# Optimization experiments

Measured on AMD Instinct MI355X. Metric: run time of the kernel, lower is better.

The kernel has to match this reference:

```python
import jax, jax.numpy as jnp
import numpy as np
import math

N, E, NF, BF, H, NH, DEPTH = 2048, 65536, 128, 16, 512, 8, 5
HD = H // NH

def _lin(key, fan_in, fan_out):
    k1, k2 = jax.random.split(key)
    W = jax.random.normal(k1, (fan_in, fan_out), jnp.float32) * math.sqrt(2.0 / fan_out)
    b = jnp.zeros((fan_out,), jnp.float32)
    return W, b

def setup_inputs() -> dict:
    key = jax.random.key(0)
    ks = jax.random.split(key, 12)
    x = jax.random.normal(ks[0], (N, NF), jnp.float32)
    edge_index = jax.random.randint(ks[1], (2, E), 0, N, jnp.int64)
    edge_attr = jax.random.normal(ks[2], (E, BF), jnp.float32)
    Wn, bn = _lin(ks[3], NF, H)
    We, be = _lin(ks[4], BF, NH)
    Wq, bq = _lin(ks[5], H, H)
    Wk, bk = _lin(ks[6], H, H)
    Wv, bv = _lin(ks[7], H, H)
    Wo, bo = _lin(ks[8], H, H)
    W1, b1 = _lin(ks[9], H, 4 * H)
    W2, b2 = _lin(ks[10], 4 * H, H)
    g1 = jnp.ones((H,), jnp.float32); be1 = jnp.zeros((H,), jnp.float32)
    g2 = jnp.ones((H,), jnp.float32); be2 = jnp.zeros((H,), jnp.float32)
    return dict(x=x, edge_index=edge_index, edge_attr=edge_attr,
                Wn=Wn, bn=bn, We=We, be=be, Wq=Wq, bq=bq, Wk=Wk, bk=bk,
                Wv=Wv, bv=bv, Wo=Wo, bo=bo, W1=W1, b1=b1, W2=W2, b2=b2,
                g1=g1, be1=be1, g2=g2, be2=be2)

def _ln(x, g, b, eps=1e-5):
    m = jnp.mean(x, axis=-1, keepdims=True)
    v = jnp.var(x, axis=-1, keepdims=True)
    return (x - m) * jax.lax.rsqrt(v + eps) * g + b

def reference(x, edge_index, edge_attr, Wn, bn, We, be, Wq, bq, Wk, bk,
              Wv, bv, Wo, bo, W1, b1, W2, b2, g1, be1, g2, be2):
    h = x @ Wn + bn                                   # [N, H]
    e_bias = edge_attr @ We + be                      # [E, NH]
    src, dst = edge_index[0], edge_index[1]
    bias = jnp.zeros((NH, N, N), jnp.float32).at[:, src, dst].set(e_bias.T)
    scale = 1.0 / math.sqrt(HD)
    for _ in range(DEPTH):
        Q = (h @ Wq + bq).reshape(N, NH, HD).transpose(1, 0, 2)   # [h, n, d]
        K = (h @ Wk + bk).reshape(N, NH, HD).transpose(1, 0, 2)
        V = (h @ Wv + bv).reshape(N, NH, HD).transpose(1, 0, 2)
        scores = jnp.einsum('hnd,hmd->hnm', Q, K) * scale + bias  # [h, n, m]
        attn = jax.nn.softmax(scores, axis=-1)
        out = jnp.einsum('hnm,hmd->hnd', attn, V)                 # [h, n, d]
        out = out.transpose(1, 0, 2).reshape(N, H) @ Wo + bo
        h = _ln(h + out, g1, be1)
        h_ff = jnp.maximum(h @ W1 + b1, 0.0) @ W2 + b2
        h = _ln(h + h_ff, g2, be2)
    return h
```

## Files before the change

### kernel.cpp

```cpp
#include <hip/hip_runtime.h>
#include <hip/hip_bf16.h>

#define NN 2048
#define EE 65536
#define NF_ 128
#define HH 512
#define NHH 8
#define HD 64
#define DEPTH 5
#define KSPLIT 2
#define KEYS_PER (NN / KSPLIT)
#define NTILE (KEYS_PER / 64)
#define NTILE_TOT (NN / 64)
#define LOG2E 1.4426950408889634f

typedef __attribute__((ext_vector_type(8))) short bf16x8;
typedef __attribute__((ext_vector_type(4))) float f32x4;

__device__ __forceinline__ ushort f2bf(float x) {
    uint u = __builtin_bit_cast(uint, x);
    u += 0x7fffu + ((u >> 16) & 1u);
    return (ushort)(u >> 16);
}

#define GLD16(gp, lp)                                                          \
    __builtin_amdgcn_global_load_lds(                                          \
        (const __attribute__((address_space(1))) unsigned int*)(gp),           \
        (__attribute__((address_space(3))) unsigned int*)(lp), 16, 0, 0)

__device__ __forceinline__ void bar_lgkm() {
    asm volatile("s_waitcnt lgkmcnt(0)" ::: "memory");
    __builtin_amdgcn_s_barrier();
    __builtin_amdgcn_sched_barrier(0);
}
__device__ __forceinline__ void bar_vm(int pk) {
    if (pk) asm volatile("s_waitcnt vmcnt(2) lgkmcnt(0)" ::: "memory");
    else    asm volatile("s_waitcnt vmcnt(0) lgkmcnt(0)" ::: "memory");
    __builtin_amdgcn_s_barrier();
    __builtin_amdgcn_sched_barrier(0);
}

template<int BM, int BN, int OUT, int RELU>
__global__ __launch_bounds__(256) void gemm_mfma(const ushort* __restrict__ A,
                                                 const ushort* __restrict__ Bt,
                                                 const float* __restrict__ bias,
                                                 float* __restrict__ C,
                                                 ushort* __restrict__ Cb,
                                                 ushort* __restrict__ qb,
                                                 ushort* __restrict__ kb,
                                                 ushort* __restrict__ vtb,
                                                 int M, int N, int K) {
    constexpr int WM = BM / 2, WN = BN / 2;
    constexpr int MR = BM / 32, NR = BN / 32;
    __shared__ __align__(16) ushort As[2][BM * 64];
    __shared__ __align__(16) ushort Bs[2][BN * 64];
    const int t = threadIdx.x;
    const int w = t >> 6, l = t & 63;
    const int wr = w >> 1, wc = w & 1;
    const int m0 = blockIdx.y * BM, n0 = blockIdx.x * BN;

    f32x4 acc[MR][NR];
#pragma unroll
    for (int m = 0; m < MR; ++m)
#pragma unroll
        for (int n = 0; n < NR; ++n) acc[m][n] = (f32x4){0.f, 0.f, 0.f, 0.f};

    const int srow = t >> 3, sch = t & 7;
    auto stage = [&](int buf, int kt) {
#pragma unroll
        for (int r = 0; r < MR; ++r) {
            int rr = r * 32 + srow;
            int c = sch ^ (rr & 7);
            GLD16(A + (size_t)(m0 + rr) * K + kt * 64 + c * 8,
                  &As[buf][rr * 64 + sch * 8]);
        }
#pragma unroll
        for (int r = 0; r < NR; ++r) {
            int rr = r * 32 + srow;
            int c = sch ^ (rr & 7);
            GLD16(Bt + (size_t)(n0 + rr) * K + kt * 64 + c * 8,
                  &Bs[buf][rr * 64 + sch * 8]);
        }
    };

    stage(0, 0);
    const int NT = K / 64;
    for (int kt = 0; kt < NT; ++kt) {
        __syncthreads();
        if (kt + 1 < NT) stage((kt + 1) & 1, kt + 1);
        const int buf = kt & 1;
#pragma unroll
        for (int kk = 0; kk < 2; ++kk) {
            bf16x8 af[MR], bfr[NR];
#pragma unroll
            for (int m = 0; m < MR; ++m) {
                int R = wr * WM + m * 16 + (l & 15);
                int c = kk * 4 + (l >> 4);
                af[m] = *(const bf16x8*)&As[buf][R * 64 + (c ^ (R & 7)) * 8];
            }
#pragma unroll
            for (int n = 0; n < NR; ++n) {
                int R = wc * WN + n * 16 + (l & 15);
                int c = kk * 4 + (l >> 4);
                bfr[n] = *(const bf16x8*)&Bs[buf][R * 64 + (c ^ (R & 7)) * 8];
            }
#pragma unroll
            for (int m = 0; m < MR; ++m)
#pragma unroll
                for (int n = 0; n < NR; ++n)
                    acc[m][n] = __builtin_amdgcn_mfma_f32_16x16x32_bf16(af[m], bfr[n], acc[m][n], 0, 0, 0);
        }
    }

#pragma unroll
    for (int m = 0; m < MR; ++m) {
        int row = m0 + wr * WM + m * 16 + (l >> 4) * 4;
#pragma unroll
        for (int n = 0; n < NR; ++n) {
            int col = n0 + wc * WN + n * 16 + (l & 15);
            float bv = bias[col];
#pragma unroll
            for (int j = 0; j < 4; ++j) {
                float vv = acc[m][n][j] + bv;
                if (RELU) vv = fmaxf(vv, 0.f);
                int r = row + j;
                if (OUT == 0) {
                    C[(size_t)r * N + col] = vv;
                } else if (OUT == 1) {
                    C[(size_t)r * N + col] = vv;
                    Cb[(size_t)r * N + col] = f2bf(vv);
                } else if (OUT == 2) {
                    Cb[(size_t)r * N + col] = f2bf(vv);
                } else {
                    int type = col >> 9, head = (col >> 6) & 7, dd = col & 63;
                    ushort bv16 = f2bf(vv);
                    if (type == 0) qb[((size_t)head * NN + r) * 64 + dd] = bv16;
                    else if (type == 1) kb[((size_t)head * NN + r) * 64 + dd] = bv16;
                    else vtb[((size_t)head * 64 + dd) * NN + r] = bv16;
                }
            }
        }
    }
}

__global__ __launch_bounds__(256) void xcvt(const float* __restrict__ x, ushort* __restrict__ xb, int n) {
    int i = blockIdx.x * 256 + threadIdx.x;
    if (i < n) xb[i] = f2bf(x[i]);
}

__global__ __launch_bounds__(256) void wtrans(const float* __restrict__ W, ushort* __restrict__ WT,
                                              int K, int N, int rowoff) {
    __shared__ float tile[32][33];
    int n0 = blockIdx.x * 32, k0 = blockIdx.y * 32;
    int tc = threadIdx.x & 31, tr = threadIdx.x >> 5;
#pragma unroll
    for (int i = 0; i < 32; i += 8) tile[tr + i][tc] = W[(size_t)(k0 + tr + i) * N + n0 + tc];
    __syncthreads();
#pragma unroll
    for (int i = 0; i < 32; i += 8)
        WT[(size_t)(rowoff + n0 + tr + i) * K + k0 + tc] = f2bf(tile[tc][tr + i]);
}

__global__ __launch_bounds__(256) void bconcat(const float* __restrict__ a, const float* __restrict__ b,
                                               const float* __restrict__ c, float* __restrict__ o) {
    int i = blockIdx.x * 256 + threadIdx.x;
    if (i < 1536) o[i] = i < 512 ? a[i] : (i < 1024 ? b[i - 512] : c[i - 1024]);
}

__global__ __launch_bounds__(256) void ebias_kernel(const float* __restrict__ ea,
                                                    const float* __restrict__ We,
                                                    const float* __restrict__ be,
                                                    float* __restrict__ eb) {
    int e = blockIdx.x * 256 + threadIdx.x;
    float a[16];
#pragma unroll
    for (int i = 0; i < 16; ++i) a[i] = ea[(size_t)e * 16 + i];
#pragma unroll
    for (int j = 0; j < 8; ++j) {
        float s = be[j];
#pragma unroll
        for (int i = 0; i < 16; ++i) s += a[i] * We[i * 8 + j];
        eb[(size_t)e * 8 + j] = s;
    }
}

__global__ __launch_bounds__(256) void amax_kernel(const int* __restrict__ eidx, int* __restrict__ lastE) {
    int e = blockIdx.x * 256 + threadIdx.x;
    int s = eidx[e], d = eidx[EE + e];
    atomicMax(&lastE[s * NN + d], e);
}

__global__ __launch_bounds__(256) void count_kernel(const int* __restrict__ eidx,
                                                    const int* __restrict__ lastE,
                                                    int* __restrict__ cnt) {
    int e = blockIdx.x * 256 + threadIdx.x;
    int s = eidx[e], d = eidx[EE + e];
    if (lastE[s * NN + d] == e) atomicAdd(&cnt[s], 1);
}

__global__ __launch_bounds__(256) void scan2048(const int* __restrict__ cnt,
                                                int* __restrict__ rowptr) {
    __shared__ int sums[256];
    int t = threadIdx.x;
    int loc[8];
    int s = 0;
#pragma unroll
    for (int i = 0; i < 8; ++i) { loc[i] = s; s += cnt[t * 8 + i]; }
    sums[t] = s;
    __syncthreads();
    for (int off = 1; off < 256; off <<= 1) {
        int v = (t >= off) ? sums[t - off] : 0;
        __syncthreads();
        sums[t] += v;
        __syncthreads();
    }
    int base = (t == 0) ? 0 : sums[t - 1];
#pragma unroll
    for (int i = 0; i < 8; ++i) rowptr[t * 8 + i] = base + loc[i];
    if (t == 255) rowptr[NN] = sums[255];
}

__global__ __launch_bounds__(256) void rt_count(const int* __restrict__ eidx,
                                                const int* __restrict__ lastE,
                                                int* __restrict__ cnt2) {
    int e = blockIdx.x * 256 + threadIdx.x;
    int s = eidx[e], d = eidx[EE + e];
    if (lastE[s * NN + d] == e) atomicAdd(&cnt2[s * NTILE_TOT + (d >> 6)], 1);
}

__global__ __launch_bounds__(256) void rt_scan(const int* __restrict__ rowptr,
                                               const int* __restrict__ cnt2,
                                               int* __restrict__ rtptr,
                                               int* __restrict__ rtoff) {
    int row = blockIdx.x * 256 + threadIdx.x;
    if (row >= NN) return;
    int base = rowptr[row];
#pragma unroll
    for (int t = 0; t < NTILE_TOT; ++t) {
        rtptr[row * NTILE_TOT + t] = base;
        rtoff[row * NTILE_TOT + t] = base;
        base += cnt2[row * NTILE_TOT + t];
    }
    if (row == NN - 1) rtptr[NN * NTILE_TOT] = base;
}

__global__ __launch_bounds__(256) void rt_fill(const int* __restrict__ eidx,
                                               const int* __restrict__ lastE,
                                               const float* __restrict__ eb,
                                               int* __restrict__ rtoff,
                                               int* __restrict__ csr_dst,
                                               float* __restrict__ csr_b) {
    int e = blockIdx.x * 256 + threadIdx.x;
    int s = eidx[e], d = eidx[EE + e];
    if (lastE[s * NN + d] == e) {
        int pos = atomicAdd(&rtoff[s * NTILE_TOT + (d >> 6)], 1);
        csr_dst[pos] = d & 63;
#pragma unroll
        for (int j = 0; j < 8; ++j) csr_b[(size_t)pos * 8 + j] = eb[(size_t)e * 8 + j] * LOG2E;
    }
}

__global__ __launch_bounds__(256) void attn_mfma(const ushort* __restrict__ qb,
                                                 const ushort* __restrict__ kb,
                                                 const ushort* __restrict__ vtb,
                                                 const int* __restrict__ rtptr,
                                                 const int* __restrict__ csr_dst,
                                                 const float* __restrict__ csr_b,
                                                 float* __restrict__ opart,
                                                 float* __restrict__ Mp,
                                                 float* __restrict__ Sp) {
    const int id = blockIdx.x;
    const int f = (id & 7) * 128 + (id >> 3);
    const int n0 = (f & 63) * 32;
    const int head = (f >> 6) & 7;
    const int ks = f >> 9;
    const int t = threadIdx.x;
    const int w = t >> 6, l = t & 63;
    const int mh = w & 1, nh = w >> 1;
    const float c1 = 0.125f * LOG2E;

    __shared__ __align__(16) ushort Ks2[2][64 * 64];
    __shared__ __align__(16) ushort Vs[64 * 64];
    __shared__ __align__(16) float  Sl[32][68];
    __shared__ __align__(16) ushort Pb[32][72];
    __shared__ float Mrow[32], Srow[32], Frow[32];
    __shared__ int Rt[32][17];

    bf16x8 qf0, qf1;
    {
        int r = n0 + mh * 16 + (l & 15);
        const ushort* qp = qb + ((size_t)head * NN + r) * HD + ((l >> 4) * 8);
        qf0 = *(const bf16x8*)qp;
        qf1 = *(const bf16x8*)(qp + 32);
    }
    if (t < 32) { Mrow[t] = -1e30f; Srow[t] = 0.f; }
    for (int i = t; i < 32 * 17; i += 256) {
        int r = i / 17, c = i % 17;
        Rt[r][c] = rtptr[(n0 + r) * NTILE_TOT + ks * NTILE + c];
    }
    const int brow = t >> 3, bj = t & 7;
    f32x4 o0 = {0.f, 0.f, 0.f, 0.f}, o1 = {0.f, 0.f, 0.f, 0.f};

    auto stageK = [&](int buf, int tile) {
        int m0k = ks * KEYS_PER + tile * 64;
#pragma unroll
        for (int s = 0; s < 2; ++s) {
            int slot = t + s * 256;
            int rr = slot >> 3, blk = slot & 7, sb = blk ^ (rr & 7);
            GLD16(kb + ((size_t)head * NN + m0k + rr) * 64 + sb * 8,
                  &Ks2[buf][rr * 64 + blk * 8]);
        }
    };
    auto stageV = [&](int tile) {
        int m0k = ks * KEYS_PER + tile * 64;
#pragma unroll
        for (int s = 0; s < 2; ++s) {
            int slot = t + s * 256;
            int rr = slot >> 3, blk = slot & 7, sb = blk ^ (rr & 7);
            GLD16(vtb + ((size_t)head * 64 + rr) * NN + m0k + sb * 8,
                  &Vs[rr * 64 + blk * 8]);
        }
    };

    stageK(0, 0);
    __syncthreads();

    for (int tt = 0; tt < NTILE; ++tt) {
        const int buf = tt & 1;
        const int pk = (tt + 1 < NTILE);
        stageV(tt);
        if (pk) stageK(buf ^ 1, tt + 1);

        {
            const ushort* Kb_ = &Ks2[buf][0];
            int db = l >> 4;
            int key0 = nh * 32 + (l & 15), key1 = key0 + 16;
            bf16x8 ka0 = *(const bf16x8*)&Kb_[key0 * 64 + ((db ^ (key0 & 7)) * 8)];
            bf16x8 ka1 = *(const bf16x8*)&Kb_[key0 * 64 + (((db + 4) ^ (key0 & 7)) * 8)];
            bf16x8 kb0 = *(const bf16x8*)&Kb_[key1 * 64 + ((db ^ (key1 & 7)) * 8)];
            bf16x8 kb1 = *(const bf16x8*)&Kb_[key1 * 64 + (((db + 4) ^ (key1 & 7)) * 8)];
            f32x4 s0 = {0.f, 0.f, 0.f, 0.f}, s1 = {0.f, 0.f, 0.f, 0.f};
            __builtin_amdgcn_s_setprio(1);
            s0 = __builtin_amdgcn_mfma_f32_16x16x32_bf16(qf0, ka0, s0, 0, 0, 0);
            s0 = __builtin_amdgcn_mfma_f32_16x16x32_bf16(qf1, ka1, s0, 0, 0, 0);
            s1 = __builtin_amdgcn_mfma_f32_16x16x32_bf16(qf0, kb0, s1, 0, 0, 0);
            s1 = __builtin_amdgcn_mfma_f32_16x16x32_bf16(qf1, kb1, s1, 0, 0, 0);
            __builtin_amdgcn_s_setprio(0);
            int row = mh * 16 + (l >> 4) * 4;
            int c0 = nh * 32 + (l & 15);
#pragma unroll
            for (int j = 0; j < 4; ++j) {
                Sl[row + j][c0] = s0[j] * c1;
                Sl[row + j][c0 + 16] = s1[j] * c1;
            }
        }
        bar_lgkm();

        {
            const int cbase = bj * 8;
            const int p0 = Rt[brow][tt], p1 = Rt[brow][tt + 1];
            for (int e = p0; e < p1; ++e) {
                int dd = csr_dst[e];
                if ((dd >> 3) == bj) Sl[brow][dd] += csr_b[(size_t)e * 8 + head];
            }
            f32x4 a = *(const f32x4*)&Sl[brow][cbase];
            f32x4 b = *(const f32x4*)&Sl[brow][cbase + 4];
            float tm = fmaxf(fmaxf(fmaxf(a[0], a[1]), fmaxf(a[2], a[3])),
                             fmaxf(fmaxf(b[0], b[1]), fmaxf(b[2], b[3])));
            tm = fmaxf(tm, __shfl_xor(tm, 1, 64));
            tm = fmaxf(tm, __shfl_xor(tm, 2, 64));
            tm = fmaxf(tm, __shfl_xor(tm, 4, 64));
            float Mo = Mrow[brow];
            float Mn = fmaxf(Mo, tm);
            float p[8];
#pragma unroll
            for (int i = 0; i < 4; ++i) p[i] = exp2f(a[i] - Mn);
#pragma unroll
            for (int i = 0; i < 4; ++i) p[4 + i] = exp2f(b[i] - Mn);
            float ts = 0.f;
#pragma unroll
            for (int i = 0; i < 8; ++i) ts += p[i];
            ts += __shfl_xor(ts, 1, 64);
            ts += __shfl_xor(ts, 2, 64);
            ts += __shfl_xor(ts, 4, 64);
            int4 pkv;
            pkv.x = (int)((uint)f2bf(p[0]) | ((uint)f2bf(p[1]) << 16));
            pkv.y = (int)((uint)f2bf(p[2]) | ((uint)f2bf(p[3]) << 16));
            pkv.z = (int)((uint)f2bf(p[4]) | ((uint)f2bf(p[5]) << 16));
            pkv.w = (int)((uint)f2bf(p[6]) | ((uint)f2bf(p[7]) << 16));
            *(int4*)&Pb[brow][cbase] = pkv;
            if (bj == 0) {
                float f_ = exp2f(Mo - Mn);
                Mrow[brow] = Mn;
                Srow[brow] = Srow[brow] * f_ + ts;
                Frow[brow] = f_;
            }
        }
        bar_vm(pk);

        {
            int row4 = mh * 16 + (l >> 4) * 4;
#pragma unroll
            for (int j = 0; j < 4; ++j) {
                float fj = Frow[row4 + j];
                o0[j] *= fj;
                o1[j] *= fj;
            }
            int kbase = (l >> 4) * 8;
            int prow = mh * 16 + (l & 15);
            bf16x8 p0 = *(const bf16x8*)&Pb[prow][kbase];
            bf16x8 p1 = *(const bf16x8*)&Pb[prow][kbase + 32];
            int kb_ = l >> 4;
            int d0 = nh * 32 + (l & 15), d1 = d0 + 16;
            bf16x8 v00 = *(const bf16x8*)&Vs[d0 * 64 + ((kb_ ^ (d0 & 7)) * 8)];
            bf16x8 v01 = *(const bf16x8*)&Vs[d0 * 64 + (((kb_ + 4) ^ (d0 & 7)) * 8)];
            bf16x8 v10 = *(const bf16x8*)&Vs[d1 * 64 + ((kb_ ^ (d1 & 7)) * 8)];
            bf16x8 v11 = *(const bf16x8*)&Vs[d1 * 64 + (((kb_ + 4) ^ (d1 & 7)) * 8)];
            __builtin_amdgcn_s_setprio(1);
            o0 = __builtin_amdgcn_mfma_f32_16x16x32_bf16(p0, v00, o0, 0, 0, 0);
            o0 = __builtin_amdgcn_mfma_f32_16x16x32_bf16(p1, v01, o0, 0, 0, 0);
            o1 = __builtin_amdgcn_mfma_f32_16x16x32_bf16(p0, v10, o1, 0, 0, 0);
            o1 = __builtin_amdgcn_mfma_f32_16x16x32_bf16(p1, v11, o1, 0, 0, 0);
            __builtin_amdgcn_s_setprio(0);
        }
        __syncthreads();
    }

    {
        int row4 = mh * 16 + (l >> 4) * 4;
        int c0 = nh * 32 + (l & 15);
#pragma unroll
        for (int j = 0; j < 4; ++j) {
            int r = row4 + j;
            float* dst = opart + ((size_t)ks * NN + n0 + r) * HH + head * HD;
            dst[c0] = o0[j];
            dst[c0 + 16] = o1[j];
        }
    }
    if (t < 32) {
        Mp[((size_t)ks * NHH + head) * NN + n0 + t] = Mrow[t];
        Sp[((size_t)ks * NHH + head) * NN + n0 + t] = Srow[t];
    }
}

__global__ __launch_bounds__(256) void attn_combine(const float* __restrict__ opart,
                                                    const float* __restrict__ Mp,
                                                    const float* __restrict__ Sp,
                                                    ushort* __restrict__ aob) {
    int i = blockIdx.x * 256 + threadIdx.x;
    int row = i >> 9, col = i & 511;
    int head = col >> 6;
    float m0 = Mp[(size_t)head * NN + row];
    float m1 = Mp[((size_t)NHH + head) * NN + row];
    float s0 = Sp[(size_t)head * NN + row];
    float s1 = Sp[((size_t)NHH + head) * NN + row];
    float m = fmaxf(m0, m1);
    float w0 = exp2f(m0 - m), w1 = exp2f(m1 - m);
    float ov0 = opart[(size_t)row * HH + col];
    float ov1 = opart[((size_t)NN + row) * HH + col];
    aob[i] = f2bf((ov0 * w0 + ov1 * w1) / (s0 * w0 + s1 * w1));
}

template<int BF16OUT>
__global__ __launch_bounds__(256) void ln_kernel(const float* __restrict__ a,
                                                 const float* __restrict__ b,
                                                 const float* __restrict__ g,
                                                 const float* __restrict__ be,
                                                 float* __restrict__ out,
                                                 ushort* __restrict__ outb) {
    int row = blockIdx.x * 4 + (threadIdx.x >> 6);
    int lane = threadIdx.x & 63;
    const float* pa = a + (size_t)row * HH;
    const float* pb = b + (size_t)row * HH;
    float x[8];
    float s = 0.f;
#pragma unroll
    for (int i = 0; i < 8; ++i) { x[i] = pa[lane + i * 64] + pb[lane + i * 64]; s += x[i]; }
#pragma unroll
    for (int off = 32; off > 0; off >>= 1) s += __shfl_xor(s, off, 64);
    float mean = s * (1.f / 512.f);
    float vs = 0.f;
#pragma unroll
    for (int i = 0; i < 8; ++i) { float d = x[i] - mean; vs += d * d; }
#pragma unroll
    for (int off = 32; off > 0; off >>= 1) vs += __shfl_xor(vs, off, 64);
    float rs = rsqrtf(vs * (1.f / 512.f) + 1e-5f);
    float* po = out + (size_t)row * HH;
    ushort* pob = outb + (size_t)row * HH;
#pragma unroll
    for (int i = 0; i < 8; ++i) {
        float v = (x[i] - mean) * rs * g[lane + i * 64] + be[lane + i * 64];
        po[lane + i * 64] = v;
        if (BF16OUT) pob[lane + i * 64] = f2bf(v);
    }
}

extern "C" void kernel_launch(void* const* d_in, const int* in_sizes, int n_in,
                              void* d_out, int out_size, void* d_ws, size_t ws_size,
                              hipStream_t stream) {
    const float* x   = (const float*)d_in[0];
    const int*  eidx = (const int*)d_in[1];
    const float* ea  = (const float*)d_in[2];
    const float* Wn = (const float*)d_in[3];  const float* bn = (const float*)d_in[4];
    const float* We = (const float*)d_in[5];  const float* be = (const float*)d_in[6];
    const float* Wq = (const float*)d_in[7];  const float* bq = (const float*)d_in[8];
    const float* Wk = (const float*)d_in[9];  const float* bk = (const float*)d_in[10];
    const float* Wv = (const float*)d_in[11]; const float* bv = (const float*)d_in[12];
    const float* Wo = (const float*)d_in[13]; const float* bo = (const float*)d_in[14];
    const float* W1 = (const float*)d_in[15]; const float* b1 = (const float*)d_in[16];
    const float* W2 = (const float*)d_in[17]; const float* b2 = (const float*)d_in[18];
    const float* g1 = (const float*)d_in[19]; const float* be1 = (const float*)d_in[20];
    const float* g2 = (const float*)d_in[21]; const float* be2 = (const float*)d_in[22];
    float* out = (float*)d_out;

    char* base = (char*)d_ws;
    size_t off = 0;
    auto carve = [&](size_t bytes) { void* p = base + off; off = (off + bytes + 255) & ~(size_t)255; return p; };
    float*  h    = (float*)carve((size_t)NN * HH * 4);
    ushort* hb   = (ushort*)carve((size_t)NN * HH * 2);
    float*  po   = (float*)carve((size_t)NN * HH * 4);
    ushort* ff1b = (ushort*)carve((size_t)NN * 4 * HH * 2);
    ushort* qb   = (ushort*)carve((size_t)NN * HH * 2);
    ushort* kbf  = (ushort*)carve((size_t)NN * HH * 2);
    ushort* vtb  = (ushort*)carve((size_t)NN * HH * 2);
    ushort* aob  = (ushort*)carve((size_t)NN * HH * 2);
    ushort* xb   = (ushort*)carve((size_t)NN * NF_ * 2);
    ushort* WnT  = (ushort*)carve((size_t)HH * NF_ * 2);
    ushort* WqkvT= (ushort*)carve((size_t)3 * HH * HH * 2);
    ushort* WoT  = (ushort*)carve((size_t)HH * HH * 2);
    ushort* W1T  = (ushort*)carve((size_t)4 * HH * HH * 2);
    ushort* W2T  = (ushort*)carve((size_t)4 * HH * HH * 2);
    float*  bqkv = (float*)carve((size_t)3 * HH * 4);
    float*  eb   = (float*)carve((size_t)EE * NHH * 4);
    float*  csr_b= (float*)carve((size_t)EE * NHH * 4);
    float*  Mp   = (float*)carve((size_t)KSPLIT * NHH * NN * 4);
    float*  Sp   = (float*)carve((size_t)KSPLIT * NHH * NN * 4);
    int* cnt     = (int*)carve((size_t)NN * 4);
    int* rowptr  = (int*)carve((size_t)(NN + 1) * 4);
    int* csr_dst = (int*)carve((size_t)EE * 4);
    int* cnt2    = (int*)carve((size_t)NN * NTILE_TOT * 4);
    int* rtptr   = (int*)carve((size_t)(NN * NTILE_TOT + 1) * 4);
    int* rtoff   = (int*)carve((size_t)NN * NTILE_TOT * 4);
    int* lastE = (int*)po;
    float* opart = (float*)ff1b;

    hipMemsetAsync(lastE, 0xFF, (size_t)NN * NN * 4, stream);
    hipMemsetAsync(cnt, 0, (size_t)NN * 4, stream);
    hipMemsetAsync(cnt2, 0, (size_t)NN * NTILE_TOT * 4, stream);

    xcvt<<<(NN * NF_ + 255) / 256, 256, 0, stream>>>(x, xb, NN * NF_);
    wtrans<<<dim3(HH / 32, NF_ / 32), 256, 0, stream>>>(Wn, WnT, NF_, HH, 0);
    wtrans<<<dim3(HH / 32, HH / 32), 256, 0, stream>>>(Wq, WqkvT, HH, HH, 0);
    wtrans<<<dim3(HH / 32, HH / 32), 256, 0, stream>>>(Wk, WqkvT, HH, HH, 512);
    wtrans<<<dim3(HH / 32, HH / 32), 256, 0, stream>>>(Wv, WqkvT, HH, HH, 1024);
    wtrans<<<dim3(HH / 32, HH / 32), 256, 0, stream>>>(Wo, WoT, HH, HH, 0);
    wtrans<<<dim3(4 * HH / 32, HH / 32), 256, 0, stream>>>(W1, W1T, HH, 4 * HH, 0);
    wtrans<<<dim3(HH / 32, 4 * HH / 32), 256, 0, stream>>>(W2, W2T, 4 * HH, HH, 0);
    bconcat<<<6, 256, 0, stream>>>(bq, bk, bv, bqkv);

    ebias_kernel<<<EE / 256, 256, 0, stream>>>(ea, We, be, eb);
    amax_kernel<<<EE / 256, 256, 0, stream>>>(eidx, lastE);
    count_kernel<<<EE / 256, 256, 0, stream>>>(eidx, lastE, cnt);
    scan2048<<<1, 256, 0, stream>>>(cnt, rowptr);
    rt_count<<<EE / 256, 256, 0, stream>>>(eidx, lastE, cnt2);
    rt_scan<<<NN / 256, 256, 0, stream>>>(rowptr, cnt2, rtptr, rtoff);
    rt_fill<<<EE / 256, 256, 0, stream>>>(eidx, lastE, eb, rtoff, csr_dst, csr_b);

    gemm_mfma<64, 64, 1, 0><<<dim3(HH / 64, NN / 64), 256, 0, stream>>>(
        xb, WnT, bn, h, hb, nullptr, nullptr, nullptr, NN, HH, NF_);

    for (int d = 0; d < DEPTH; ++d) {
        gemm_mfma<128, 64, 3, 0><<<dim3(3 * HH / 64, NN / 128), 256, 0, stream>>>(
            hb, WqkvT, bqkv, nullptr, nullptr, qb, kbf, vtb, NN, 3 * HH, HH);
        attn_mfma<<<dim3(1024), 256, 0, stream>>>(
            qb, kbf, vtb, rtptr, csr_dst, csr_b, opart, Mp, Sp);
        attn_combine<<<NN * HH / 256, 256, 0, stream>>>(opart, Mp, Sp, aob);
        gemm_mfma<32, 64, 0, 0><<<dim3(HH / 64, NN / 32), 256, 0, stream>>>(
            aob, WoT, bo, po, nullptr, nullptr, nullptr, nullptr, NN, HH, HH);
        ln_kernel<1><<<NN / 4, 256, 0, stream>>>(h, po, g1, be1, h, hb);
        gemm_mfma<128, 64, 2, 1><<<dim3(4 * HH / 64, NN / 128), 256, 0, stream>>>(
            hb, W1T, b1, nullptr, ff1b, nullptr, nullptr, nullptr, NN, 4 * HH, HH);
        gemm_mfma<32, 64, 0, 0><<<dim3(HH / 64, NN / 32), 256, 0, stream>>>(
            ff1b, W2T, b2, po, nullptr, nullptr, nullptr, nullptr, NN, HH, 4 * HH);
        float* dst = (d == DEPTH - 1) ? out : h;
        ln_kernel<1><<<NN / 4, 256, 0, stream>>>(h, po, g2, be2, dst, hb);
    }
    (void)in_sizes; (void)n_in; (void)out_size; (void)ws_size;
}
```

Before: 640.8 us.

## Restructure attention to per-wave softmax in registers with 64-row tiles and 3-way key split

The attention kernel now gives each block 64 query rows, with each wave owning 16 rows. The softmax runs entirely in registers from the transposed QK^T MFMA output, which removes the shared score buffer and the block-wide barriers between score, softmax and PV phases. V is now double-buffered alongside K. The key split goes from 2 to 3 chunks of uneven tile counts, and the combine kernel merges three partials, with opart moved to the po buffer. The edge-bias loop now runs per lane over a whole row, and the grid shrinks to 768 blocks, so load balance across CUs may change.

```diff
diff --git a/kernel.cpp b/kernel.cpp
--- a/kernel.cpp
+++ b/kernel.cpp
@@ -8,13 +8,12 @@
 #define NHH 8
 #define HD 64
 #define DEPTH 5
-#define KSPLIT 2
-#define KEYS_PER (NN / KSPLIT)
-#define NTILE (KEYS_PER / 64)
+#define KSPLIT 3
 #define NTILE_TOT (NN / 64)
 #define LOG2E 1.4426950408889634f
 
 typedef __attribute__((ext_vector_type(8))) short bf16x8;
+typedef __attribute__((ext_vector_type(4))) short bf16x4;
 typedef __attribute__((ext_vector_type(4))) float f32x4;
 
 __device__ __forceinline__ ushort f2bf(float x) {
@@ -27,18 +26,6 @@
     __builtin_amdgcn_global_load_lds(                                          \
         (const __attribute__((address_space(1))) unsigned int*)(gp),           \
         (__attribute__((address_space(3))) unsigned int*)(lp), 16, 0, 0)
-
-__device__ __forceinline__ void bar_lgkm() {
-    asm volatile("s_waitcnt lgkmcnt(0)" ::: "memory");
-    __builtin_amdgcn_s_barrier();
-    __builtin_amdgcn_sched_barrier(0);
-}
-__device__ __forceinline__ void bar_vm(int pk) {
-    if (pk) asm volatile("s_waitcnt vmcnt(2) lgkmcnt(0)" ::: "memory");
-    else    asm volatile("s_waitcnt vmcnt(0) lgkmcnt(0)" ::: "memory");
-    __builtin_amdgcn_s_barrier();
-    __builtin_amdgcn_sched_barrier(0);
-}
 
 template<int BM, int BN, int OUT, int RELU>
 __global__ __launch_bounds__(256) void gemm_mfma(const ushort* __restrict__ A,
@@ -270,39 +257,40 @@
                                                  float* __restrict__ Mp,
                                                  float* __restrict__ Sp) {
     const int id = blockIdx.x;
-    const int f = (id & 7) * 128 + (id >> 3);
-    const int n0 = (f & 63) * 32;
-    const int head = (f >> 6) & 7;
-    const int ks = f >> 9;
+    const int f = (id & 7) * 96 + (id >> 3);
+    const int n0 = (f & 31) * 64;
+    const int head = (f >> 5) & 7;
+    const int ks = f >> 8;
+    const int tstart = (ks * 32) / 3, tend = ((ks + 1) * 32) / 3;
     const int t = threadIdx.x;
     const int w = t >> 6, l = t & 63;
-    const int mh = w & 1, nh = w >> 1;
+    const int lq = l & 15, lg = l >> 4;
     const float c1 = 0.125f * LOG2E;
 
     __shared__ __align__(16) ushort Ks2[2][64 * 64];
-    __shared__ __align__(16) ushort Vs[64 * 64];
-    __shared__ __align__(16) float  Sl[32][68];
-    __shared__ __align__(16) ushort Pb[32][72];
-    __shared__ float Mrow[32], Srow[32], Frow[32];
-    __shared__ int Rt[32][17];
+    __shared__ __align__(16) ushort Vs2[2][64 * 64];
+    __shared__ __align__(16) ushort Pb[4][16][72];
+    __shared__ int Rt[64][12];
 
     bf16x8 qf0, qf1;
     {
-        int r = n0 + mh * 16 + (l & 15);
-        const ushort* qp = qb + ((size_t)head * NN + r) * HD + ((l >> 4) * 8);
+        int r = n0 + w * 16 + lq;
+        const ushort* qp = qb + ((size_t)head * NN + r) * HD + lg * 8;
         qf0 = *(const bf16x8*)qp;
         qf1 = *(const bf16x8*)(qp + 32);
     }
-    if (t < 32) { Mrow[t] = -1e30f; Srow[t] = 0.f; }
-    for (int i = t; i < 32 * 17; i += 256) {
-        int r = i / 17, c = i % 17;
-        Rt[r][c] = rtptr[(n0 + r) * NTILE_TOT + ks * NTILE + c];
-    }
-    const int brow = t >> 3, bj = t & 7;
-    f32x4 o0 = {0.f, 0.f, 0.f, 0.f}, o1 = {0.f, 0.f, 0.f, 0.f};
+    const int ntile = tend - tstart;
+    for (int i = t; i < 64 * 12; i += 256) {
+        int r = i / 12, c = i % 12;
+        if (c <= ntile) Rt[r][c] = rtptr[(n0 + r) * NTILE_TOT + tstart + c];
+    }
+    float M = -1e30f, S = 0.f;
+    f32x4 o[4];
+#pragma unroll
+    for (int db = 0; db < 4; ++db) o[db] = (f32x4){0.f, 0.f, 0.f, 0.f};
 
     auto stageK = [&](int buf, int tile) {
-        int m0k = ks * KEYS_PER + tile * 64;
+        int m0k = tile * 64;
 #pragma unroll
         for (int s = 0; s < 2; ++s) {
             int slot = t + s * 256;
@@ -311,135 +299,135 @@
                   &Ks2[buf][rr * 64 + blk * 8]);
         }
     };
-    auto stageV = [&](int tile) {
-        int m0k = ks * KEYS_PER + tile * 64;
+    auto stageV = [&](int buf, int tile) {
+        int m0k = tile * 64;
 #pragma unroll
         for (int s = 0; s < 2; ++s) {
             int slot = t + s * 256;
             int rr = slot >> 3, blk = slot & 7, sb = blk ^ (rr & 7);
             GLD16(vtb + ((size_t)head * 64 + rr) * NN + m0k + sb * 8,
-                  &Vs[rr * 64 + blk * 8]);
+                  &Vs2[buf][rr * 64 + blk * 8]);
         }
     };
 
-    stageK(0, 0);
+    stageK(0, tstart);
+    stageV(0, tstart);
     __syncthreads();
 
-    for (int tt = 0; tt < NTILE; ++tt) {
-        const int buf = tt & 1;
-        const int pk = (tt + 1 < NTILE);
-        stageV(tt);
-        if (pk) stageK(buf ^ 1, tt + 1);
-
+    for (int tt = tstart; tt < tend; ++tt) {
+        const int tl = tt - tstart;
+        const int cb = tl & 1;
+        if (tt + 1 < tend) { stageK(cb ^ 1, tt + 1); stageV(cb ^ 1, tt + 1); }
+
+        f32x4 vv[4];
         {
-            const ushort* Kb_ = &Ks2[buf][0];
-            int db = l >> 4;
-            int key0 = nh * 32 + (l & 15), key1 = key0 + 16;
-            bf16x8 ka0 = *(const bf16x8*)&Kb_[key0 * 64 + ((db ^ (key0 & 7)) * 8)];
-            bf16x8 ka1 = *(const bf16x8*)&Kb_[key0 * 64 + (((db + 4) ^ (key0 & 7)) * 8)];
-            bf16x8 kb0 = *(const bf16x8*)&Kb_[key1 * 64 + ((db ^ (key1 & 7)) * 8)];
-            bf16x8 kb1 = *(const bf16x8*)&Kb_[key1 * 64 + (((db + 4) ^ (key1 & 7)) * 8)];
-            f32x4 s0 = {0.f, 0.f, 0.f, 0.f}, s1 = {0.f, 0.f, 0.f, 0.f};
+            const ushort* Kb_ = &Ks2[cb][0];
             __builtin_amdgcn_s_setprio(1);
-            s0 = __builtin_amdgcn_mfma_f32_16x16x32_bf16(qf0, ka0, s0, 0, 0, 0);
-            s0 = __builtin_amdgcn_mfma_f32_16x16x32_bf16(qf1, ka1, s0, 0, 0, 0);
-            s1 = __builtin_amdgcn_mfma_f32_16x16x32_bf16(qf0, kb0, s1, 0, 0, 0);
-            s1 = __builtin_amdgcn_mfma_f32_16x16x32_bf16(qf1, kb1, s1, 0, 0, 0);
+#pragma unroll
+            for (int b = 0; b < 4; ++b) {
+                int key = b * 16 + lq;
+                bf16x8 k0 = *(const bf16x8*)&Kb_[key * 64 + ((lg ^ (key & 7)) * 8)];
+                bf16x8 k1 = *(const bf16x8*)&Kb_[key * 64 + (((lg + 4) ^ (key & 7)) * 8)];
+                f32x4 s_ = {0.f, 0.f, 0.f, 0.f};
+                s_ = __builtin_amdgcn_mfma_f32_16x16x32_bf16(k0, qf0, s_, 0, 0, 0);
+                s_ = __builtin_amdgcn_mfma_f32_16x16x32_bf16(k1, qf1, s_, 0, 0, 0);
+                vv[b] = s_;
+            }
             __builtin_amdgcn_s_setprio(0);
-            int row = mh * 16 + (l >> 4) * 4;
-            int c0 = nh * 32 + (l & 15);
-#pragma unroll
-            for (int j = 0; j < 4; ++j) {
-                Sl[row + j][c0] = s0[j] * c1;
-                Sl[row + j][c0 + 16] = s1[j] * c1;
-            }
-        }
-        bar_lgkm();
+        }
+#pragma unroll
+        for (int b = 0; b < 4; ++b)
+#pragma unroll
+            for (int j = 0; j < 4; ++j) vv[b][j] *= c1;
 
         {
-            const int cbase = bj * 8;
-            const int p0 = Rt[brow][tt], p1 = Rt[brow][tt + 1];
+            int rq = w * 16 + lq;
+            int p0 = Rt[rq][tl], p1 = Rt[rq][tl + 1];
             for (int e = p0; e < p1; ++e) {
                 int dd = csr_dst[e];
-                if ((dd >> 3) == bj) Sl[brow][dd] += csr_b[(size_t)e * 8 + head];
-            }
-            f32x4 a = *(const f32x4*)&Sl[brow][cbase];
-            f32x4 b = *(const f32x4*)&Sl[brow][cbase + 4];
-            float tm = fmaxf(fmaxf(fmaxf(a[0], a[1]), fmaxf(a[2], a[3])),
-                             fmaxf(fmaxf(b[0], b[1]), fmaxf(b[2], b[3])));
-            tm = fmaxf(tm, __shfl_xor(tm, 1, 64));
-            tm = fmaxf(tm, __shfl_xor(tm, 2, 64));
-            tm = fmaxf(tm, __shfl_xor(tm, 4, 64));
-            float Mo = Mrow[brow];
-            float Mn = fmaxf(Mo, tm);
-            float p[8];
-#pragma unroll
-            for (int i = 0; i < 4; ++i) p[i] = exp2f(a[i] - Mn);
-#pragma unroll
-            for (int i = 0; i < 4; ++i) p[4 + i] = exp2f(b[i] - Mn);
-            float ts = 0.f;
-#pragma unroll
-            for (int i = 0; i < 8; ++i) ts += p[i];
-            ts += __shfl_xor(ts, 1, 64);
-            ts += __shfl_xor(ts, 2, 64);
-            ts += __shfl_xor(ts, 4, 64);
-            int4 pkv;
-            pkv.x = (int)((uint)f2bf(p[0]) | ((uint)f2bf(p[1]) << 16));
-            pkv.y = (int)((uint)f2bf(p[2]) | ((uint)f2bf(p[3]) << 16));
-            pkv.z = (int)((uint)f2bf(p[4]) | ((uint)f2bf(p[5]) << 16));
-            pkv.w = (int)((uint)f2bf(p[6]) | ((uint)f2bf(p[7]) << 16));
-            *(int4*)&Pb[brow][cbase] = pkv;
-            if (bj == 0) {
-                float f_ = exp2f(Mo - Mn);
-                Mrow[brow] = Mn;
-                Srow[brow] = Srow[brow] * f_ + ts;
-                Frow[brow] = f_;
-            }
-        }
-        bar_vm(pk);
+                if (((dd >> 2) & 3) == lg) {
+                    float bv = csr_b[(size_t)e * 8 + head];
+#pragma unroll
+                    for (int b = 0; b < 4; ++b)
+#pragma unroll
+                        for (int j = 0; j < 4; ++j)
+                            vv[b][j] += (b == (dd >> 4) && j == (dd & 3)) ? bv : 0.f;
+                }
+            }
+        }
+
+        float mx = vv[0][0];
+#pragma unroll
+        for (int b = 0; b < 4; ++b)
+#pragma unroll
+            for (int j = 0; j < 4; ++j) mx = fmaxf(mx, vv[b][j]);
+        mx = fmaxf(mx, __shfl_xor(mx, 16, 64));
+        mx = fmaxf(mx, __shfl_xor(mx, 32, 64));
+        float Mn = fmaxf(M, mx);
+        float fr = exp2f(M - Mn);
+        float ts = 0.f;
+#pragma unroll
+        for (int b = 0; b < 4; ++b)
+#pragma unroll
+            for (int j = 0; j < 4; ++j) { vv[b][j] = exp2f(vv[b][j] - Mn); ts += vv[b][j]; }
+        ts += __shfl_xor(ts, 16, 64);
+        ts += __shfl_xor(ts, 32, 64);
+        S = S * fr + ts;
+        M = Mn;
+
+#pragma unroll
+        for (int b = 0; b < 4; ++b) {
+            uint2 pk2;
+            pk2.x = (uint)f2bf(vv[b][0]) | ((uint)f2bf(vv[b][1]) << 16);
+            pk2.y = (uint)f2bf(vv[b][2]) | ((uint)f2bf(vv[b][3]) << 16);
+            *(uint2*)&Pb[w][lq][b * 16 + lg * 4] = pk2;
+        }
+#pragma unroll
+        for (int j = 0; j < 4; ++j) {
+            float Fj = __shfl(fr, lg * 4 + j, 64);
+            o[0][j] *= Fj; o[1][j] *= Fj; o[2][j] *= Fj; o[3][j] *= Fj;
+        }
+        asm volatile("s_waitcnt lgkmcnt(0)" ::: "memory");
+        __builtin_amdgcn_sched_barrier(0);
 
         {
-            int row4 = mh * 16 + (l >> 4) * 4;
-#pragma unroll
-            for (int j = 0; j < 4; ++j) {
-                float fj = Frow[row4 + j];
-                o0[j] *= fj;
-                o1[j] *= fj;
-            }
-            int kbase = (l >> 4) * 8;
-            int prow = mh * 16 + (l & 15);
-            bf16x8 p0 = *(const bf16x8*)&Pb[prow][kbase];
-            bf16x8 p1 = *(const bf16x8*)&Pb[prow][kbase + 32];
-            int kb_ = l >> 4;
-            int d0 = nh * 32 + (l & 15), d1 = d0 + 16;
-            bf16x8 v00 = *(const bf16x8*)&Vs[d0 * 64 + ((kb_ ^ (d0 & 7)) * 8)];
-            bf16x8 v01 = *(const bf16x8*)&Vs[d0 * 64 + (((kb_ + 4) ^ (d0 & 7)) * 8)];
-            bf16x8 v10 = *(const bf16x8*)&Vs[d1 * 64 + ((kb_ ^ (d1 & 7)) * 8)];
-            bf16x8 v11 = *(const bf16x8*)&Vs[d1 * 64 + (((kb_ + 4) ^ (d1 & 7)) * 8)];
+            const ushort* pp = &Pb[w][lq][0];
+            bf16x4 a0l = *(const bf16x4*)&pp[lg * 8];
+            bf16x4 a0h = *(const bf16x4*)&pp[lg * 8 + 4];
+            bf16x4 a1l = *(const bf16x4*)&pp[32 + lg * 8];
+            bf16x4 a1h = *(const bf16x4*)&pp[32 + lg * 8 + 4];
+            bf16x8 pa0, pa1;
+#pragma unroll
+            for (int i = 0; i < 4; ++i) {
+                pa0[i] = a0l[i]; pa0[i + 4] = a0h[i];
+                pa1[i] = a1l[i]; pa1[i + 4] = a1h[i];
+            }
+            const ushort* Vb_ = &Vs2[cb][0];
             __builtin_amdgcn_s_setprio(1);
-            o0 = __builtin_amdgcn_mfma_f32_16x16x32_bf16(p0, v00, o0, 0, 0, 0);
-            o0 = __builtin_amdgcn_mfma_f32_16x16x32_bf16(p1, v01, o0, 0, 0, 0);
-            o1 = __builtin_amdgcn_mfma_f32_16x16x32_bf16(p0, v10, o1, 0, 0, 0);
-            o1 = __builtin_amdgcn_mfma_f32_16x16x32_bf16(p1, v11, o1, 0, 0, 0);
+#pragma unroll
+            for (int db = 0; db < 4; ++db) {
+                int dim = db * 16 + lq;
+                bf16x8 v0 = *(const bf16x8*)&Vb_[dim * 64 + ((lg ^ (dim & 7)) * 8)];
+                bf16x8 v1 = *(const bf16x8*)&Vb_[dim * 64 + (((lg + 4) ^ (dim & 7)) * 8)];
+                o[db] = __builtin_amdgcn_mfma_f32_16x16x32_bf16(pa0, v0, o[db], 0, 0, 0);
+                o[db] = __builtin_amdgcn_mfma_f32_16x16x32_bf16(pa1, v1, o[db], 0, 0, 0);
+            }
             __builtin_amdgcn_s_setprio(0);
         }
         __syncthreads();
     }
 
-    {
-        int row4 = mh * 16 + (l >> 4) * 4;
-        int c0 = nh * 32 + (l & 15);
+#pragma unroll
+    for (int db = 0; db < 4; ++db)
 #pragma unroll
         for (int j = 0; j < 4; ++j) {
-            int r = row4 + j;
-            float* dst = opart + ((size_t)ks * NN + n0 + r) * HH + head * HD;
-            dst[c0] = o0[j];
-            dst[c0 + 16] = o1[j];
-        }
-    }
-    if (t < 32) {
-        Mp[((size_t)ks * NHH + head) * NN + n0 + t] = Mrow[t];
-        Sp[((size_t)ks * NHH + head) * NN + n0 + t] = Srow[t];
+            int r = n0 + w * 16 + lg * 4 + j;
+            opart[((size_t)ks * NN + r) * HH + head * HD + db * 16 + lq] = o[db][j];
+        }
+    if (l < 16) {
+        int r = n0 + w * 16 + l;
+        Mp[((size_t)ks * NHH + head) * NN + r] = M;
+        Sp[((size_t)ks * NHH + head) * NN + r] = S;
     }
 }
 
@@ -452,13 +440,17 @@
     int head = col >> 6;
     float m0 = Mp[(size_t)head * NN + row];
     float m1 = Mp[((size_t)NHH + head) * NN + row];
+    float m2 = Mp[((size_t)2 * NHH + head) * NN + row];
     float s0 = Sp[(size_t)head * NN + row];
     float s1 = Sp[((size_t)NHH + head) * NN + row];
-    float m = fmaxf(m0, m1);
-    float w0 = exp2f(m0 - m), w1 = exp2f(m1 - m);
-    float ov0 = opart[(size_t)row * HH + col];
-    float ov1 = opart[((size_t)NN + row) * HH + col];
-    aob[i] = f2bf((ov0 * w0 + ov1 * w1) / (s0 * w0 + s1 * w1));
+    float s2 = Sp[((size_t)2 * NHH + head) * NN + row];
+    float m = fmaxf(m0, fmaxf(m1, m2));
+    float w0 = exp2f(m0 - m), w1 = exp2f(m1 - m), w2 = exp2f(m2 - m);
+    float num = opart[(size_t)row * HH + col] * w0
+              + opart[((size_t)NN + row) * HH + col] * w1
+              + opart[((size_t)2 * NN + row) * HH + col] * w2;
+    float den = s0 * w0 + s1 * w1 + s2 * w2;
+    aob[i] = f2bf(num / den);
 }
 
 template<int BF16OUT>
@@ -542,7 +534,7 @@
     int* rtptr   = (int*)carve((size_t)(NN * NTILE_TOT + 1) * 4);
     int* rtoff   = (int*)carve((size_t)NN * NTILE_TOT * 4);
     int* lastE = (int*)po;
-    float* opart = (float*)ff1b;
+    float* opart = (float*)po;
 
     hipMemsetAsync(lastE, 0xFF, (size_t)NN * NN * 4, stream);
     hipMemsetAsync(cnt, 0, (size_t)NN * 4, stream);
@@ -572,7 +564,7 @@
     for (int d = 0; d < DEPTH; ++d) {
         gemm_mfma<128, 64, 3, 0><<<dim3(3 * HH / 64, NN / 128), 256, 0, stream>>>(
             hb, WqkvT, bqkv, nullptr, nullptr, qb, kbf, vtb, NN, 3 * HH, HH);
-        attn_mfma<<<dim3(1024), 256, 0, stream>>>(
+        attn_mfma<<<dim3(32 * NHH * KSPLIT), 256, 0, stream>>>(
             qb, kbf, vtb, rtptr, csr_dst, csr_b, opart, Mp, Sp);
         attn_combine<<<NN * HH / 256, 256, 0, stream>>>(opart, Mp, Sp, aob);
         gemm_mfma<32, 64, 0, 0><<<dim3(HH / 64, NN / 32), 256, 0, stream>>>(
```

Result: slower. 655.6 us (+2.3%).
